# Kernel tuning notes

Hardware: AMD Instinct MI355X
Metric: run time of the kernel (lower is better)

## Reference

```python
import jax, jax.numpy as jnp
import numpy as np

D_MODEL = 1024
NUM_HEADS = 16
D_K = D_MODEL // NUM_HEADS
ROPE_THETA = 10000.0


def apply_rope(x, positions):
    # x: (b, h, s, d_k), positions: (b, s) int
    half = D_K // 2
    inv_freq = ROPE_THETA ** (-jnp.arange(half, dtype=jnp.float32) * 2.0 / D_K)  # (half,)
    angles = positions[:, None, :, None].astype(jnp.float32) * inv_freq  # (b,1,s,half)
    cos, sin = jnp.cos(angles), jnp.sin(angles)
    x_even = x[..., 0::2]
    x_odd = x[..., 1::2]
    r_even = x_even * cos - x_odd * sin
    r_odd = x_even * sin + x_odd * cos
    # re-interleave
    out = jnp.stack([r_even, r_odd], axis=-1).reshape(x.shape)
    return out


def setup_inputs() -> dict:
    key = jax.random.key(0)
    k1, k2, k3, k4, k5 = jax.random.split(key, 5)
    b, s = 2, 2048
    scale = 1.0 / np.sqrt(D_MODEL)
    x = jax.random.normal(k1, (b, s, D_MODEL), dtype=jnp.float32)
    w_q = jax.random.normal(k2, (D_MODEL, D_MODEL), dtype=jnp.float32) * scale
    w_k = jax.random.normal(k3, (D_MODEL, D_MODEL), dtype=jnp.float32) * scale
    w_v = jax.random.normal(k4, (D_MODEL, D_MODEL), dtype=jnp.float32) * scale
    w_o = jax.random.normal(k5, (D_MODEL, D_MODEL), dtype=jnp.float32) * scale
    token_positions = jnp.broadcast_to(jnp.arange(s, dtype=jnp.int64 if jax.config.jax_enable_x64 else jnp.int32), (b, s))
    return {"x": x, "w_q": w_q, "w_k": w_k, "w_v": w_v, "w_o": w_o,
            "token_positions": token_positions}


def reference(x, w_q, w_k, w_v, w_o, token_positions):
    b, s, _ = x.shape
    # QKV projections: w_* are (h*d_k, d_model); y = x @ w^T
    def proj(w):
        y = jnp.einsum('bsd,ed->bse', x, w)  # (b,s,h*d_k)
        return y.reshape(b, s, NUM_HEADS, D_K).transpose(0, 2, 1, 3)  # (b,h,s,d_k)
    Q, K, V = proj(w_q), proj(w_k), proj(w_v)
    Q = apply_rope(Q, token_positions)
    K = apply_rope(K, token_positions)
    scores = jnp.einsum('bhqd,bhkd->bhqk', Q, K) / jnp.sqrt(jnp.float32(D_K))
    causal = jnp.tril(jnp.ones((s, s), dtype=bool))
    scores = jnp.where(causal[None, None], scores, -jnp.inf)
    attn = jax.nn.softmax(scores, axis=-1)
    out = jnp.einsum('bhqk,bhkd->bhqd', attn, V)  # (b,h,s,d_v)
    out = out.transpose(0, 2, 1, 3).reshape(b, s, NUM_HEADS * D_K)
    return jnp.einsum('bse,de->bsd', out, w_o)
```

## Files before the change

### kernel.cpp

```cpp
#include <hip/hip_runtime.h>

#define B_ 2
#define S_ 2048
#define DM 1024
#define NH 16
#define DK 64

using bf16x8  = __attribute__((ext_vector_type(8)))  short;
using f32x4   = __attribute__((ext_vector_type(4)))  float;

__device__ __forceinline__ float bf2f(short v){
  unsigned u = ((unsigned)(unsigned short)v) << 16;
  union { unsigned u; float f; } c; c.u = u; return c.f;
}
__device__ __forceinline__ short f2bf(float f){
  union { float f; unsigned u; } c; c.f = f;
  unsigned u = c.u + 0x7FFFu + ((c.u >> 16) & 1u);
  return (short)(u >> 16);
}
__device__ __forceinline__ unsigned packbf(float lo, float hi){
  union { float f; unsigned u; } a, b; a.f = lo; b.f = hi;
  return __builtin_amdgcn_perm(b.u, a.u, 0x07060302u);
}
__device__ __forceinline__ void gload16(const void* g, void* l){
  __builtin_amdgcn_global_load_lds(
    (const __attribute__((address_space(1))) unsigned*)g,
    (__attribute__((address_space(3))) unsigned*)l, 16, 0, 0);
}

__global__ void cast_rope(const float* __restrict__ x, const float* __restrict__ wq,
                          const float* __restrict__ wk, const float* __restrict__ wv,
                          const float* __restrict__ wo, const int* __restrict__ pos,
                          short* __restrict__ xb, short* __restrict__ wqkv,
                          short* __restrict__ wob, float* __restrict__ tab){
  const int bid = blockIdx.x;
  if (bid < 8192){
    int i = bid * 256 + threadIdx.x;
    const float4* src; short4* dst;
    if (i < (1 << 20)){
      src = (const float4*)x + i; dst = (short4*)xb + i;
    } else {
      int j = i - (1 << 20);
      int seg = j >> 18, off = j & ((1 << 18) - 1);
      const float* sp = seg == 0 ? wq : seg == 1 ? wk : seg == 2 ? wv : wo;
      short* dp = seg < 3 ? wqkv + ((size_t)seg << 20) : wob;
      src = (const float4*)sp + off; dst = (short4*)dp + off;
    }
    float4 v = *src;
    short4 o; o.x = f2bf(v.x); o.y = f2bf(v.y); o.z = f2bf(v.z); o.w = f2bf(v.w);
    *dst = o;
  } else {
    int idx = (bid - 8192) * 256 + threadIdx.x;
    int j = idx & 31, bs = idx >> 5;
    float p = (float)pos[bs];
    float inv = powf(10000.0f, -(float)(2 * j) / 64.0f);
    float ang = p * inv;
    tab[(size_t)bs * 64 + j]      = cosf(ang);
    tab[(size_t)bs * 64 + 32 + j] = sinf(ang);
  }
}

__launch_bounds__(512)
__global__ void gemm_qkv(const short* __restrict__ A, const short* __restrict__ Bm,
                         const float* __restrict__ tab,
                         short* __restrict__ Qr, short* __restrict__ Kr,
                         short* __restrict__ Vt){
  __shared__ short lds[3 * 8192];
  constexpr int K = 1024, NT = 32;
  const int tid = threadIdx.x;
  const int l = tid & 63, w = tid >> 6;
  const int lr = l & 15, lg = l >> 4;
  const int wr = w >> 2, wc = w & 3;
  const int nwg = gridDim.x * gridDim.y;
  const int wg  = blockIdx.y * gridDim.x + blockIdx.x;
  const int sw  = (wg & 7) * (nwg >> 3) + (wg >> 3);
  const int bn  = sw % gridDim.x, bm = sw / gridDim.x;
  const short* Ab = A  + (size_t)bm * 128 * K;
  const short* Bb = Bm + (size_t)bn * 128 * K;
  const int r0 = tid >> 2, c4 = tid & 3;
  f32x4 acc[4][2];
  #pragma unroll
  for (int m = 0; m < 4; ++m)
    #pragma unroll
    for (int n = 0; n < 2; ++n) acc[m][n] = (f32x4){0.f, 0.f, 0.f, 0.f};

  auto stage = [&](int t){
    short* buf = lds + (t % 3) * 8192;
    gload16(Ab + (size_t)r0 * K + t * 32 + c4 * 8, buf + tid * 8);
    gload16(Bb + (size_t)r0 * K + t * 32 + c4 * 8, buf + 4096 + tid * 8);
  };

  stage(0); stage(1);
  for (int t = 0; t < NT; ++t){
    if (t < NT - 1) asm volatile("s_waitcnt vmcnt(2)" ::: "memory");
    else            asm volatile("s_waitcnt vmcnt(0)" ::: "memory");
    __builtin_amdgcn_s_barrier();
    __builtin_amdgcn_sched_barrier(0);
    if (t + 2 < NT) stage(t + 2);
    const short* bufA = lds + (t % 3) * 8192;
    const short* bufB = bufA + 4096;
    bf16x8 a[4], bfr[2];
    #pragma unroll
    for (int m = 0; m < 4; ++m)
      a[m] = *(const bf16x8*)(bufA + (wr * 64 + m * 16 + lr) * 32 + lg * 8);
    #pragma unroll
    for (int n = 0; n < 2; ++n)
      bfr[n] = *(const bf16x8*)(bufB + (wc * 32 + n * 16 + lr) * 32 + lg * 8);
    __builtin_amdgcn_s_setprio(1);
    #pragma unroll
    for (int m = 0; m < 4; ++m)
      #pragma unroll
      for (int n = 0; n < 2; ++n)
        acc[m][n] = __builtin_amdgcn_mfma_f32_16x16x32_bf16(a[m], bfr[n], acc[m][n], 0, 0, 0);
    __builtin_amdgcn_s_setprio(0);
  }

  if (bn >= 16){
    __syncthreads();
    short* T = lds;
    #pragma unroll
    for (int m = 0; m < 4; ++m)
      #pragma unroll
      for (int n = 0; n < 2; ++n){
        const int col_l = wc * 32 + n * 16 + lr;
        const int row0  = wr * 64 + m * 16 + lg * 4;
        short4 pk;
        pk.x = f2bf(acc[m][n][0]); pk.y = f2bf(acc[m][n][1]);
        pk.z = f2bf(acc[m][n][2]); pk.w = f2bf(acc[m][n][3]);
        *(short4*)(T + col_l * 136 + row0) = pk;
      }
    __syncthreads();
    const int h0   = (bn - 16) * 2;
    const int tok0 = bm * 128;
    const int b    = tok0 >> 11, s0 = tok0 & 2047;
    const int col_l = tid >> 2;
    const int d  = col_l & 63;
    const int hh = h0 + (col_l >> 6);
    short* dstrow = Vt + ((size_t)(b * NH + hh) * DK + d) * S_ + s0;
    #pragma unroll
    for (int k = 0; k < 4; ++k){
      const int chunk = (tid & 3) * 4 + k;
      bf16x8 v = *(const bf16x8*)(T + col_l * 136 + chunk * 8);
      *(bf16x8*)(dstrow + chunk * 8) = v;
    }
  } else {
    #pragma unroll
    for (int m = 0; m < 4; ++m)
      #pragma unroll
      for (int n = 0; n < 2; ++n){
        const int col = bn * 128 + wc * 32 + n * 16 + lr;
        const int which = col >> 10;
        #pragma unroll
        for (int j = 0; j < 4; ++j){
          const int row = bm * 128 + wr * 64 + m * 16 + lg * 4 + j;
          float v = acc[m][n][j];
          const int d  = col & 63;
          const int dp = d >> 1;
          const float c = tab[(size_t)row * 64 + dp];
          const float s = tab[(size_t)row * 64 + 32 + dp];
          const float p = __shfl_xor(v, 1);
          float r = v * c + p * ((d & 1) ? s : -s);
          if (which == 0) r *= 0.125f;
          short* dst = which ? Kr : Qr;
          const int b = row >> 11, si = row & 2047;
          const int h = (col >> 6) & 15;
          dst[(((size_t)(b * NH + h)) * S_ + si) * DK + d] = f2bf(r);
        }
      }
  }
}

__launch_bounds__(512)
__global__ void gemm_o(const short* __restrict__ A, const short* __restrict__ Bm,
                       float* __restrict__ C){
  __shared__ short As[128 * 32];
  __shared__ short Bs[64 * 32];
  constexpr int K = 1024, N = 1024;
  const int tid = threadIdx.x;
  const int l = tid & 63, w = tid >> 6;
  const int lr = l & 15, lg = l >> 4;
  const int wr = w >> 2, wc = w & 3;
  const int nwg = gridDim.x * gridDim.y;
  const int wg  = blockIdx.y * gridDim.x + blockIdx.x;
  const int sw  = (wg & 7) * (nwg >> 3) + (wg >> 3);
  const int bn  = sw % gridDim.x, bm = sw / gridDim.x;
  const short* Ab = A  + (size_t)bm * 128 * K;
  const short* Bb = Bm + (size_t)bn * 64 * K;
  f32x4 acc[4];
  #pragma unroll
  for (int m = 0; m < 4; ++m) acc[m] = (f32x4){0.f, 0.f, 0.f, 0.f};
  const int r0 = tid >> 2, c4 = tid & 3;
  for (int kt = 0; kt < K; kt += 32){
    gload16(Ab + (size_t)r0 * K + kt + c4 * 8, As + tid * 8);
    if (tid < 256)
      gload16(Bb + (size_t)r0 * K + kt + c4 * 8, Bs + tid * 8);
    __syncthreads();
    bf16x8 a[4], bfr;
    #pragma unroll
    for (int m = 0; m < 4; ++m)
      a[m] = *(const bf16x8*)(As + (wr * 64 + m * 16 + lr) * 32 + lg * 8);
    bfr = *(const bf16x8*)(Bs + (wc * 16 + lr) * 32 + lg * 8);
    #pragma unroll
    for (int m = 0; m < 4; ++m)
      acc[m] = __builtin_amdgcn_mfma_f32_16x16x32_bf16(a[m], bfr, acc[m], 0, 0, 0);
    __syncthreads();
  }
  #pragma unroll
  for (int m = 0; m < 4; ++m)
    #pragma unroll
    for (int j = 0; j < 4; ++j){
      int row = bm * 128 + wr * 64 + m * 16 + lg * 4 + j;
      int col = bn * 64 + wc * 16 + lr;
      C[(size_t)row * N + col] = acc[m][j];
    }
}

__device__ __forceinline__ void attn_tile_step(
    const bf16x8 qa0, const bf16x8 qa1,
    f32x4 (&acc)[4], float& mrow, float& lsum,
    const short* Ks, const short* Vs, unsigned* pw,
    int diagmask, int lr, int lg, int wl){
  float sv[4][4];
  #pragma unroll
  for (int n = 0; n < 4; ++n){
    const int R = n * 16 + lr;
    const int c0 = lg ^ (R & 7);
    bf16x8 k0 = *(const bf16x8*)(Ks + R * 64 + c0 * 8);
    bf16x8 k1 = *(const bf16x8*)(Ks + R * 64 + (c0 ^ 4) * 8);
    f32x4 z = (f32x4){0.f, 0.f, 0.f, 0.f};
    z = __builtin_amdgcn_mfma_f32_16x16x32_bf16(k0, qa0, z, 0, 0, 0);
    z = __builtin_amdgcn_mfma_f32_16x16x32_bf16(k1, qa1, z, 0, 0, 0);
    #pragma unroll
    for (int j = 0; j < 4; ++j) sv[n][j] = z[j];
  }
  if (diagmask){
    const int qloc = wl * 16 + lr;
    #pragma unroll
    for (int n = 0; n < 4; ++n)
      #pragma unroll
      for (int j = 0; j < 4; ++j)
        if (n * 16 + lg * 4 + j > qloc) sv[n][j] = -1e30f;
  }
  float lm = sv[0][0];
  #pragma unroll
  for (int n = 0; n < 4; ++n)
    #pragma unroll
    for (int j = 0; j < 4; ++j) lm = fmaxf(lm, sv[n][j]);
  lm = fmaxf(lm, __shfl_xor(lm, 16));
  lm = fmaxf(lm, __shfl_xor(lm, 32));
  if (!__all(lm <= mrow + 8.f)){
    float mnew = fmaxf(mrow, lm);
    float corr = __expf(mrow - mnew);
    mrow = mnew;
    lsum *= corr;
    float cb[4];
    #pragma unroll
    for (int j = 0; j < 4; ++j) cb[j] = __shfl(corr, lg * 4 + j);
    #pragma unroll
    for (int n = 0; n < 4; ++n)
      #pragma unroll
      for (int j = 0; j < 4; ++j) acc[n][j] *= cb[j];
  }
  float psum = 0.f;
  #pragma unroll
  for (int n = 0; n < 4; ++n)
    #pragma unroll
    for (int j = 0; j < 4; ++j){
      float p = __expf(sv[n][j] - mrow);
      sv[n][j] = p; psum += p;
    }
  psum += __shfl_xor(psum, 16);
  psum += __shfl_xor(psum, 32);
  lsum += psum;
  const int swz = (lr & 7) << 2;
  #pragma unroll
  for (int n = 0; n < 4; ++n){
    pw[lr * 32 + ((n * 8 + lg * 2 + 0) ^ swz)] = packbf(sv[n][0], sv[n][1]);
    pw[lr * 32 + ((n * 8 + lg * 2 + 1) ^ swz)] = packbf(sv[n][2], sv[n][3]);
  }
  bf16x8 pa0 = *(const bf16x8*)(pw + lr * 32 + ((lg * 4) ^ swz));
  bf16x8 pa1 = *(const bf16x8*)(pw + lr * 32 + ((16 + lg * 4) ^ swz));
  #pragma unroll
  for (int n = 0; n < 4; ++n){
    const int R = n * 16 + lr;
    const int c0 = lg ^ (R & 7);
    bf16x8 v0 = *(const bf16x8*)(Vs + R * 64 + c0 * 8);
    bf16x8 v1 = *(const bf16x8*)(Vs + R * 64 + (c0 ^ 4) * 8);
    acc[n] = __builtin_amdgcn_mfma_f32_16x16x32_bf16(pa0, v0, acc[n], 0, 0, 0);
    acc[n] = __builtin_amdgcn_mfma_f32_16x16x32_bf16(pa1, v1, acc[n], 0, 0, 0);
  }
}

__launch_bounds__(512)
__global__ void attn_kernel(const short* __restrict__ Qr, const short* __restrict__ Kr,
                            const short* __restrict__ Vt, short* __restrict__ AO){
  __shared__ short Ks[2][64 * 64];
  __shared__ short Vs[2][64 * 64];
  __shared__ unsigned Pw[8][16 * 32];
  const int tid = threadIdx.x;
  const int l = tid & 63, w = tid >> 6;
  const int lr = l & 15, lg = l >> 4;
  const int wl = w & 3, wgp = w >> 2;
  const int bid = blockIdx.x;
  const int qp = bid >> 5;
  const int bh = (((bid >> 3) & 3) << 3) | (bid & 7);
  const int h = bh & 15, b = bh >> 4;
  const int t0 = qp, t1 = 31 - qp;
  const int myqt = wgp ? t0 : t1;
  const short* Qp = Qr + (size_t)bh * S_ * DK;
  const short* Kp = Kr + (size_t)bh * S_ * DK;
  const short* Vp = Vt + (size_t)bh * DK * S_;

  bf16x8 qa0, qa1;
  {
    const short* q0 = Qp + (size_t)(myqt * 64 + wl * 16 + lr) * DK + lg * 8;
    qa0 = *(const bf16x8*)q0; qa1 = *(const bf16x8*)(q0 + 32);
  }
  f32x4 acc[4];
  float ms = -1e30f, ls = 0.f;
  #pragma unroll
  for (int n = 0; n < 4; ++n) acc[n] = (f32x4){0.f, 0.f, 0.f, 0.f};
  unsigned* pw = &Pw[w][0];
  const int r0 = tid >> 3, q8 = tid & 7;
  const int sq8 = q8 ^ (r0 & 7);

  gload16(Kp + (size_t)r0 * DK + sq8 * 8, &Ks[0][tid * 8]);
  gload16(Vp + (size_t)r0 * S_ + sq8 * 8, &Vs[0][tid * 8]);
  int cur = 0;
  for (int kt = 0; kt <= t1; ++kt){
    __syncthreads();
    if (kt < t1){
      gload16(Kp + (size_t)((kt + 1) * 64 + r0) * DK + sq8 * 8, &Ks[cur ^ 1][tid * 8]);
      gload16(Vp + (size_t)r0 * S_ + (kt + 1) * 64 + sq8 * 8,   &Vs[cur ^ 1][tid * 8]);
    }
    if (kt <= myqt)
      attn_tile_step(qa0, qa1, acc, ms, ls, Ks[cur], Vs[cur], pw, kt == myqt, lr, lg, wl);
    cur ^= 1;
  }
  const float li = 1.f / ls;
  #pragma unroll
  for (int j = 0; j < 4; ++j){
    const float d0 = __shfl(li, lg * 4 + j);
    #pragma unroll
    for (int n = 0; n < 4; ++n){
      int e = h * 64 + n * 16 + lr;
      int r = myqt * 64 + wl * 16 + lg * 4 + j;
      AO[((size_t)b * S_ + r) * DM + e] = f2bf(acc[n][j] * d0);
    }
  }
}

extern "C" void kernel_launch(void* const* d_in, const int* in_sizes, int n_in,
                              void* d_out, int out_size, void* d_ws, size_t ws_size,
                              hipStream_t stream){
  const float* x  = (const float*)d_in[0];
  const float* wq = (const float*)d_in[1];
  const float* wk = (const float*)d_in[2];
  const float* wv = (const float*)d_in[3];
  const float* wo = (const float*)d_in[4];
  const int*  pos = (const int*)d_in[5];

  char* ws = (char*)d_ws;
  short* xb   = (short*)(ws + 0);
  short* wqkv = (short*)(ws + ((size_t)8  << 20));
  short* wob  = (short*)(ws + ((size_t)14 << 20));
  short* Qr   = (short*)(ws + ((size_t)40 << 20));
  short* Kr   = (short*)(ws + ((size_t)48 << 20));
  short* Vt   = (short*)(ws + ((size_t)56 << 20));
  float* tab  = (float*)(ws + ((size_t)64 << 20));
  short* AO   = xb;
  float* out  = (float*)d_out;

  cast_rope<<<dim3(8704), dim3(256), 0, stream>>>(x, wq, wk, wv, wo, pos, xb, wqkv, wob, tab);
  gemm_qkv<<<dim3(24, 32), dim3(512), 0, stream>>>(xb, wqkv, tab, Qr, Kr, Vt);
  attn_kernel<<<dim3(512), dim3(512), 0, stream>>>(Qr, Kr, Vt, AO);
  gemm_o<<<dim3(16, 32), dim3(512), 0, stream>>>(AO, wob, out);
}
```

Baseline: 114.8 us.

## Split attention blocks into one query tile each, scheduled longest first

The attention kernel used 512-thread blocks, each handling a short and a long causal query tile with half its waves. It now launches 1024 blocks of 256 threads, each owning a single query tile, with the longest tiles dispatched first. Each thread issues two K and two V async loads per tile to fill the shared buffers. This removes waves that sat idle in barriers once their short tile finished, and gives the scheduler finer blocks to balance. Total K/V traffic stays about the same, but load balance now depends on hardware block dispatch order rather than explicit pairing.

```diff
diff --git a/kernel.cpp b/kernel.cpp
--- a/kernel.cpp
+++ b/kernel.cpp
@@ -291,29 +291,27 @@
   }
 }
 
-__launch_bounds__(512)
+__launch_bounds__(256)
 __global__ void attn_kernel(const short* __restrict__ Qr, const short* __restrict__ Kr,
                             const short* __restrict__ Vt, short* __restrict__ AO){
   __shared__ short Ks[2][64 * 64];
   __shared__ short Vs[2][64 * 64];
-  __shared__ unsigned Pw[8][16 * 32];
+  __shared__ unsigned Pw[4][16 * 32];
   const int tid = threadIdx.x;
   const int l = tid & 63, w = tid >> 6;
   const int lr = l & 15, lg = l >> 4;
-  const int wl = w & 3, wgp = w >> 2;
   const int bid = blockIdx.x;
-  const int qp = bid >> 5;
+  const int qo = bid >> 5;
+  const int qt = 31 - qo;
   const int bh = (((bid >> 3) & 3) << 3) | (bid & 7);
   const int h = bh & 15, b = bh >> 4;
-  const int t0 = qp, t1 = 31 - qp;
-  const int myqt = wgp ? t0 : t1;
   const short* Qp = Qr + (size_t)bh * S_ * DK;
   const short* Kp = Kr + (size_t)bh * S_ * DK;
   const short* Vp = Vt + (size_t)bh * DK * S_;
 
   bf16x8 qa0, qa1;
   {
-    const short* q0 = Qp + (size_t)(myqt * 64 + wl * 16 + lr) * DK + lg * 8;
+    const short* q0 = Qp + (size_t)(qt * 64 + w * 16 + lr) * DK + lg * 8;
     qa0 = *(const bf16x8*)q0; qa1 = *(const bf16x8*)(q0 + 32);
   }
   f32x4 acc[4];
@@ -324,17 +322,26 @@
   const int r0 = tid >> 3, q8 = tid & 7;
   const int sq8 = q8 ^ (r0 & 7);
 
-  gload16(Kp + (size_t)r0 * DK + sq8 * 8, &Ks[0][tid * 8]);
-  gload16(Vp + (size_t)r0 * S_ + sq8 * 8, &Vs[0][tid * 8]);
+  {
+    const short* kb = Kp + (size_t)r0 * DK + sq8 * 8;
+    gload16(kb,           &Ks[0][tid * 8]);
+    gload16(kb + 32 * DK, &Ks[0][(tid + 256) * 8]);
+    const short* vb = Vp + (size_t)r0 * S_ + sq8 * 8;
+    gload16(vb,           &Vs[0][tid * 8]);
+    gload16(vb + 32 * S_, &Vs[0][(tid + 256) * 8]);
+  }
   int cur = 0;
-  for (int kt = 0; kt <= t1; ++kt){
-    __syncthreads();
-    if (kt < t1){
-      gload16(Kp + (size_t)((kt + 1) * 64 + r0) * DK + sq8 * 8, &Ks[cur ^ 1][tid * 8]);
-      gload16(Vp + (size_t)r0 * S_ + (kt + 1) * 64 + sq8 * 8,   &Vs[cur ^ 1][tid * 8]);
-    }
-    if (kt <= myqt)
-      attn_tile_step(qa0, qa1, acc, ms, ls, Ks[cur], Vs[cur], pw, kt == myqt, lr, lg, wl);
+  for (int kt = 0; kt <= qt; ++kt){
+    __syncthreads();
+    if (kt < qt){
+      const short* kb = Kp + (size_t)((kt + 1) * 64 + r0) * DK + sq8 * 8;
+      gload16(kb,           &Ks[cur ^ 1][tid * 8]);
+      gload16(kb + 32 * DK, &Ks[cur ^ 1][(tid + 256) * 8]);
+      const short* vb = Vp + (size_t)r0 * S_ + (kt + 1) * 64 + sq8 * 8;
+      gload16(vb,           &Vs[cur ^ 1][tid * 8]);
+      gload16(vb + 32 * S_, &Vs[cur ^ 1][(tid + 256) * 8]);
+    }
+    attn_tile_step(qa0, qa1, acc, ms, ls, Ks[cur], Vs[cur], pw, kt == qt, lr, lg, w);
     cur ^= 1;
   }
   const float li = 1.f / ls;
@@ -344,7 +351,7 @@
     #pragma unroll
     for (int n = 0; n < 4; ++n){
       int e = h * 64 + n * 16 + lr;
-      int r = myqt * 64 + wl * 16 + lg * 4 + j;
+      int r = qt * 64 + w * 16 + lg * 4 + j;
       AO[((size_t)b * S_ + r) * DM + e] = f2bf(acc[n][j] * d0);
     }
   }
@@ -373,6 +380,6 @@
 
   cast_rope<<<dim3(8704), dim3(256), 0, stream>>>(x, wq, wk, wv, wo, pos, xb, wqkv, wob, tab);
   gemm_qkv<<<dim3(24, 32), dim3(512), 0, stream>>>(xb, wqkv, tab, Qr, Kr, Vt);
-  attn_kernel<<<dim3(512), dim3(512), 0, stream>>>(Qr, Kr, Vt, AO);
+  attn_kernel<<<dim3(1024), dim3(256), 0, stream>>>(Qr, Kr, Vt, AO);
   gemm_o<<<dim3(16, 32), dim3(512), 0, stream>>>(AO, wob, out);
 }
```

After: 116.6 us. Within noise of the previous version (+1.6%).
